# Kernel tuning notes

Hardware: AMD Instinct MI355X
Metric: run time of the kernel (lower is better)

Reference implementation:

```python
import jax, jax.numpy as jnp
import numpy as np

D_MODEL = 1024
SEQ = 4096
BATCH = 4


def _rope_cos_sin(m, d, dtype=jnp.float32):
    # Faithful to source: theta = 10000 ** (-2*(i-1)/d)  (note the i-1, as in the torch code)
    i = jnp.arange(d // 2, dtype=jnp.float32)
    theta = 10000.0 ** (-2.0 * (i - 1.0) / d)          # [d/2]
    ang = jnp.arange(m, dtype=jnp.float32)[:, None] * theta[None, :]  # [m, d/2]
    return jnp.cos(ang).astype(dtype), jnp.sin(ang).astype(dtype)


def _rotate(t, cos, sin):
    # t: [b, m, d]. Equivalent to (t @ R[pos]) with the source's block-diagonal R:
    # out[2i]   =  t[2i]*cos + t[2i+1]*sin
    # out[2i+1] = -t[2i]*sin + t[2i+1]*cos
    b, m, d = t.shape
    t2 = t.reshape(b, m, d // 2, 2)
    e, o = t2[..., 0], t2[..., 1]
    out = jnp.stack([e * cos + o * sin, -e * sin + o * cos], axis=-1)
    return out.reshape(b, m, d)


def setup_inputs() -> dict:
    key = jax.random.key(0)
    kx, kq, kk, kv = jax.random.split(key, 4)
    s = 1.0 / np.sqrt(D_MODEL)
    return {
        "x": jax.random.normal(kx, (BATCH, SEQ, D_MODEL), dtype=jnp.float32),
        "w_q": jax.random.normal(kq, (D_MODEL, D_MODEL), dtype=jnp.float32) * s,
        "w_k": jax.random.normal(kk, (D_MODEL, D_MODEL), dtype=jnp.float32) * s,
        "w_v": jax.random.normal(kv, (D_MODEL, D_MODEL), dtype=jnp.float32) * s,
    }


def reference(x, w_q, w_k, w_v):
    b, m, d = x.shape
    q = x @ w_q.T  # nn.Linear: y = x W^T
    k = x @ w_k.T
    v = x @ w_v.T
    cos, sin = _rope_cos_sin(m, d, x.dtype)
    q_rot = _rotate(q, cos, sin)
    k_rot = _rotate(k, cos, sin)
    # causal scaled dot-product attention (dropout disabled for deterministic reference)
    scale = 1.0 / jnp.sqrt(jnp.asarray(d, x.dtype))
    scores = jnp.einsum('bqd,bkd->bqk', q_rot, k_rot) * scale  # [b, m, m]
    causal = jnp.tril(jnp.ones((m, m), dtype=bool))
    scores = jnp.where(causal[None], scores, jnp.asarray(-jnp.inf, x.dtype))
    weights = jax.nn.softmax(scores, axis=-1)
    return jnp.einsum('bqk,bkd->bqd', weights, v)
```

## Files before the change

### kernel.cpp

```cpp
#include <hip/hip_runtime.h>

#define BATCH 4
#define SEQ 4096
#define DM 1024
#define HALF_D 512
#define NROWS (BATCH * SEQ)
#define NT128 528
#define TILE_ELE 16384

typedef _Float16 f16x8 __attribute__((ext_vector_type(8)));
typedef _Float16 f16x4 __attribute__((ext_vector_type(4)));
typedef _Float16 f16x2 __attribute__((ext_vector_type(2)));
typedef float f32x4 __attribute__((ext_vector_type(4)));

#define AS1(p) ((const __attribute__((address_space(1))) void*)(p))
#define AS3(p) ((__attribute__((address_space(3))) void*)(p))

__global__ __launch_bounds__(256) void cvt_f32_f16(
    const float* __restrict__ src, _Float16* __restrict__ dst, int n8) {
  int i = blockIdx.x * 256 + threadIdx.x;
  if (i >= n8) return;
  const float4* s = (const float4*)src;
  float4 a = s[2 * i], b = s[2 * i + 1];
  f16x8 h;
  h[0] = (_Float16)a.x; h[1] = (_Float16)a.y;
  h[2] = (_Float16)a.z; h[3] = (_Float16)a.w;
  h[4] = (_Float16)b.x; h[5] = (_Float16)b.y;
  h[6] = (_Float16)b.z; h[7] = (_Float16)b.w;
  *(f16x8*)&dst[8 * i] = h;
}

__global__ __launch_bounds__(256) void rope_apply(_Float16* __restrict__ T) {
  int idx = blockIdx.x * 256 + threadIdx.x;
  int row = idx >> 9;
  int i = idx & 511;
  int pos = row & (SEQ - 1);
  float theta = expf(-0.017988946039016f * ((float)i - 1.0f));
  float ang = (float)pos * theta;
  float c = cosf(ang), s = sinf(ang);
  f16x2 p = ((f16x2*)T)[idx];
  float e = (float)p[0], o = (float)p[1];
  p[0] = (_Float16)(e * c + o * s);
  p[1] = (_Float16)(o * c - e * s);
  ((f16x2*)T)[idx] = p;
}

template <int MODE>
__global__ __launch_bounds__(256) void gemm128(
    const _Float16* __restrict__ A, const _Float16* __restrict__ B,
    void* __restrict__ Cv, int K, int lda, int ldb, int ldc,
    long long strideA, long long strideB, long long strideC) {
  int bx = blockIdx.x, bz = blockIdx.z;
  int by = (MODE == 2) ? (31 - blockIdx.y) : blockIdx.y;
  if (MODE == 1 && bx > by) return;
  A += (size_t)bz * strideA;
  B += (size_t)bz * strideB;

  __shared__ __align__(16) _Float16 sA[128 * 64];
  __shared__ __align__(16) _Float16 sB[128 * 64];

  const int tid = threadIdx.x;
  const int lane = tid & 63, wave = tid >> 6;
  const int wm = (wave & 1) * 64, wn = (wave >> 1) * 64;
  const int r16 = lane & 15, quad = lane >> 4;
  const int m0 = by * 128, n0 = bx * 128;
  const int triBase = by * (by + 1) / 2;

  f32x4 acc[4][4] = {};

  const int nkt = (MODE == 2) ? (by + 1) * 2 : (K >> 6);

  for (int kt = 0; kt < nkt; ++kt) {
#pragma unroll
    for (int j = 0; j < 4; ++j) {
      int c = j * 256 + tid;
      int row = c >> 3, col = c & 7;
      const _Float16* gA;
      if (MODE == 2) {
        gA = A + (size_t)(triBase + (kt >> 1)) * TILE_ELE + row * 128 +
             (kt & 1) * 64 + col * 8;
      } else {
        gA = A + (size_t)(m0 + row) * lda + kt * 64 + col * 8;
      }
      const _Float16* gB = B + (size_t)(n0 + row) * ldb + kt * 64 + col * 8;
      __builtin_amdgcn_global_load_lds(AS1(gA), AS3(&sA[(j * 256 + wave * 64) * 8]), 16, 0, 0);
      __builtin_amdgcn_global_load_lds(AS1(gB), AS3(&sB[(j * 256 + wave * 64) * 8]), 16, 0, 0);
    }
    __syncthreads();

#pragma unroll
    for (int ks = 0; ks < 2; ++ks) {
      f16x8 af[4], bf[4];
#pragma unroll
      for (int i = 0; i < 4; ++i) {
        af[i] = *(const f16x8*)&sA[(wm + i * 16 + r16) * 64 + ks * 32 + quad * 8];
        bf[i] = *(const f16x8*)&sB[(wn + i * 16 + r16) * 64 + ks * 32 + quad * 8];
      }
#pragma unroll
      for (int mi = 0; mi < 4; ++mi)
#pragma unroll
        for (int ni = 0; ni < 4; ++ni)
          acc[mi][ni] = __builtin_amdgcn_mfma_f32_16x16x32_f16(
              af[mi], bf[ni], acc[mi][ni], 0, 0, 0);
    }
    __syncthreads();
  }

  if (MODE == 0) {
    _Float16* C = (_Float16*)Cv;
#pragma unroll
    for (int mi = 0; mi < 4; ++mi)
#pragma unroll
      for (int ni = 0; ni < 4; ++ni)
#pragma unroll
        for (int r = 0; r < 4; ++r) {
          int grow = m0 + wm + mi * 16 + quad * 4 + r;
          int gcol = n0 + wn + ni * 16 + r16;
          C[(size_t)grow * ldc + gcol] = (_Float16)acc[mi][ni][r];
        }
  } else if (MODE == 1) {
    _Float16* C = (_Float16*)Cv + (size_t)bz * strideC +
                  (size_t)(triBase + bx) * TILE_ELE;
#pragma unroll
    for (int mi = 0; mi < 4; ++mi)
#pragma unroll
      for (int ni = 0; ni < 4; ++ni)
#pragma unroll
        for (int r = 0; r < 4; ++r) {
          int lr = wm + mi * 16 + quad * 4 + r;
          int lc = wn + ni * 16 + r16;
          C[lr * 128 + lc] = (_Float16)(acc[mi][ni][r] * 0.03125f);
        }
  } else if (MODE == 2) {
    float* C = (float*)Cv + (size_t)bz * strideC;
#pragma unroll
    for (int mi = 0; mi < 4; ++mi)
#pragma unroll
      for (int ni = 0; ni < 4; ++ni)
#pragma unroll
        for (int r = 0; r < 4; ++r) {
          int grow = m0 + wm + mi * 16 + quad * 4 + r;
          int gcol = n0 + wn + ni * 16 + r16;
          C[(size_t)grow * ldc + gcol] = acc[mi][ni][r];
        }
  } else {
    _Float16* C = (_Float16*)Cv;
#pragma unroll
    for (int mi = 0; mi < 4; ++mi)
#pragma unroll
      for (int ni = 0; ni < 4; ++ni) {
        int gcol = n0 + wn + ni * 16 + r16;
        int growb = m0 + wm + mi * 16 + quad * 4;
        int b = growb >> 12;
        int m = growb & (SEQ - 1);
        f16x4 t;
#pragma unroll
        for (int r = 0; r < 4; ++r) t[r] = (_Float16)acc[mi][ni][r];
        *(f16x4*)&C[((size_t)b * DM + gcol) * SEQ + m] = t;
      }
  }
}

__global__ __launch_bounds__(256) void softmax_rows(_Float16* __restrict__ Sp) {
  __shared__ float vals[SEQ];
  __shared__ float red[256];
  int row = blockIdx.x;
  int b = row >> 12;
  int q = row & (SEQ - 1);
  int i = q >> 7, r = q & 127;
  _Float16* base = Sp + (size_t)b * ((size_t)NT128 * TILE_ELE) +
                   (size_t)(i * (i + 1) / 2) * TILE_ELE + (size_t)r * 128;
  int tid = threadIdx.x;
  int Kv = q + 1;
  float m = -__builtin_inff();
  for (int kb = tid * 8; kb + 8 <= Kv; kb += 2048) {
    f16x8 v8 = *(const f16x8*)&base[(kb >> 7) * TILE_ELE + (kb & 127)];
#pragma unroll
    for (int t = 0; t < 8; ++t) {
      float v = (float)v8[t];
      vals[kb + t] = v;
      m = fmaxf(m, v);
    }
  }
  if (tid == 0) {
    for (int k = Kv & ~7; k < Kv; ++k) {
      float v = (float)base[(k >> 7) * TILE_ELE + (k & 127)];
      vals[k] = v;
      m = fmaxf(m, v);
    }
  }
  red[tid] = m;
  __syncthreads();
  for (int s = 128; s > 0; s >>= 1) {
    if (tid < s) red[tid] = fmaxf(red[tid], red[tid + s]);
    __syncthreads();
  }
  m = red[0];
  __syncthreads();
  float l = 0.f;
  for (int k = tid; k < Kv; k += 256) {
    float e = __expf(vals[k] - m);
    vals[k] = e;
    l += e;
  }
  red[tid] = l;
  __syncthreads();
  for (int s = 128; s > 0; s >>= 1) {
    if (tid < s) red[tid] += red[tid + s];
    __syncthreads();
  }
  float inv = 1.0f / red[0];
  int Kend = (i + 1) * 128;
  for (int kb = tid * 8; kb < Kend; kb += 2048) {
    f16x8 p;
#pragma unroll
    for (int t = 0; t < 8; ++t) {
      int k = kb + t;
      p[t] = (k < Kv) ? (_Float16)(vals[k] * inv) : (_Float16)0.f;
    }
    *(f16x8*)&base[(kb >> 7) * TILE_ELE + (kb & 127)] = p;
  }
}

extern "C" void kernel_launch(void* const* d_in, const int* in_sizes, int n_in,
                              void* d_out, int out_size, void* d_ws,
                              size_t ws_size, hipStream_t stream) {
  const float* x = (const float*)d_in[0];
  const float* wq = (const float*)d_in[1];
  const float* wk = (const float*)d_in[2];
  const float* wv = (const float*)d_in[3];
  float* out = (float*)d_out;

  char* ws = (char*)d_ws;
  _Float16* Sp = (_Float16*)ws;
  _Float16* xh = (_Float16*)ws;
  _Float16* wqh = (_Float16*)(ws + 33554432);
  _Float16* wkh = wqh + (size_t)DM * DM;
  _Float16* wvh = wkh + (size_t)DM * DM;
  _Float16* vth = (_Float16*)(ws + 69206016);
  _Float16* qh = (_Float16*)d_out;
  _Float16* kh = qh + (size_t)NROWS * DM;
  (void)ws_size; (void)in_sizes; (void)n_in; (void)out_size;

  cvt_f32_f16<<<8192, 256, 0, stream>>>(x, xh, NROWS * DM / 8);
  cvt_f32_f16<<<512, 256, 0, stream>>>(wq, wqh, DM * DM / 8);
  cvt_f32_f16<<<512, 256, 0, stream>>>(wk, wkh, DM * DM / 8);
  cvt_f32_f16<<<512, 256, 0, stream>>>(wv, wvh, DM * DM / 8);

  dim3 g0(DM / 128, NROWS / 128, 1);
  gemm128<0><<<g0, 256, 0, stream>>>(xh, wqh, qh, DM, DM, DM, DM, 0, 0, 0);
  gemm128<0><<<g0, 256, 0, stream>>>(xh, wkh, kh, DM, DM, DM, DM, 0, 0, 0);
  gemm128<3><<<g0, 256, 0, stream>>>(xh, wvh, vth, DM, DM, DM, 0, 0, 0, 0);

  rope_apply<<<NROWS * HALF_D / 256, 256, 0, stream>>>(qh);
  rope_apply<<<NROWS * HALF_D / 256, 256, 0, stream>>>(kh);

  gemm128<1><<<dim3(SEQ / 128, SEQ / 128, BATCH), 256, 0, stream>>>(
      qh, kh, Sp, DM, DM, DM, 128, (long long)SEQ * DM, (long long)SEQ * DM,
      (long long)NT128 * TILE_ELE);

  softmax_rows<<<NROWS, 256, 0, stream>>>(Sp);

  gemm128<2><<<dim3(DM / 128, SEQ / 128, BATCH), 256, 0, stream>>>(
      Sp, vth, out, SEQ, 0, SEQ, DM, (long long)NT128 * TILE_ELE,
      (long long)DM * SEQ, (long long)SEQ * DM);
}
```

Measured before the change: 699.5 us.

## Register-prefetch GEMM tiles with XOR-swizzled LDS and compact triangular grid

Replaces direct global-to-LDS loads with register-staged loads. The next k-tile is fetched into registers while MFMAs run on the current tile, so global latency overlaps compute. LDS writes and reads use an XOR swizzle of the 16-byte chunk index to avoid bank conflicts on the fragment reads. The causal QK^T launch now maps a 1D block index to lower-triangle tiles instead of launching a full grid and exiting half the blocks. The cost is more registers per thread, which may lower occupancy.

```diff
diff --git a/kernel.cpp b/kernel.cpp
--- a/kernel.cpp
+++ b/kernel.cpp
@@ -12,9 +12,6 @@
 typedef _Float16 f16x4 __attribute__((ext_vector_type(4)));
 typedef _Float16 f16x2 __attribute__((ext_vector_type(2)));
 typedef float f32x4 __attribute__((ext_vector_type(4)));
-
-#define AS1(p) ((const __attribute__((address_space(1))) void*)(p))
-#define AS3(p) ((__attribute__((address_space(3))) void*)(p))
 
 __global__ __launch_bounds__(256) void cvt_f32_f16(
     const float* __restrict__ src, _Float16* __restrict__ dst, int n8) {
@@ -50,9 +47,18 @@
     const _Float16* __restrict__ A, const _Float16* __restrict__ B,
     void* __restrict__ Cv, int K, int lda, int ldb, int ldc,
     long long strideA, long long strideB, long long strideC) {
-  int bx = blockIdx.x, bz = blockIdx.z;
-  int by = (MODE == 2) ? (31 - blockIdx.y) : blockIdx.y;
-  if (MODE == 1 && bx > by) return;
+  int bx, by;
+  if (MODE == 1) {
+    int t = blockIdx.x;
+    by = (int)((sqrtf(8.0f * (float)t + 1.0f) - 1.0f) * 0.5f);
+    while ((by + 1) * (by + 2) / 2 <= t) ++by;
+    while (by * (by + 1) / 2 > t) --by;
+    bx = t - by * (by + 1) / 2;
+  } else {
+    bx = blockIdx.x;
+    by = (MODE == 2) ? (31 - blockIdx.y) : blockIdx.y;
+  }
+  int bz = blockIdx.z;
   A += (size_t)bz * strideA;
   B += (size_t)bz * strideB;
 
@@ -67,10 +73,11 @@
   const int triBase = by * (by + 1) / 2;
 
   f32x4 acc[4][4] = {};
+  int4 ra[4], rb[4];
 
   const int nkt = (MODE == 2) ? (by + 1) * 2 : (K >> 6);
 
-  for (int kt = 0; kt < nkt; ++kt) {
+  auto gload = [&](int kt) {
 #pragma unroll
     for (int j = 0; j < 4; ++j) {
       int c = j * 256 + tid;
@@ -83,18 +90,34 @@
         gA = A + (size_t)(m0 + row) * lda + kt * 64 + col * 8;
       }
       const _Float16* gB = B + (size_t)(n0 + row) * ldb + kt * 64 + col * 8;
-      __builtin_amdgcn_global_load_lds(AS1(gA), AS3(&sA[(j * 256 + wave * 64) * 8]), 16, 0, 0);
-      __builtin_amdgcn_global_load_lds(AS1(gB), AS3(&sB[(j * 256 + wave * 64) * 8]), 16, 0, 0);
-    }
-    __syncthreads();
+      ra[j] = *(const int4*)gA;
+      rb[j] = *(const int4*)gB;
+    }
+  };
+
+  gload(0);
+  for (int kt = 0; kt < nkt; ++kt) {
+#pragma unroll
+    for (int j = 0; j < 4; ++j) {
+      int c = j * 256 + tid;
+      int row = c >> 3, col = c & 7;
+      int lofs = row * 64 + ((col ^ (row & 7)) * 8);
+      *(int4*)&sA[lofs] = ra[j];
+      *(int4*)&sB[lofs] = rb[j];
+    }
+    __syncthreads();
+    if (kt + 1 < nkt) gload(kt + 1);
 
 #pragma unroll
     for (int ks = 0; ks < 2; ++ks) {
       f16x8 af[4], bf[4];
 #pragma unroll
       for (int i = 0; i < 4; ++i) {
-        af[i] = *(const f16x8*)&sA[(wm + i * 16 + r16) * 64 + ks * 32 + quad * 8];
-        bf[i] = *(const f16x8*)&sB[(wn + i * 16 + r16) * 64 + ks * 32 + quad * 8];
+        int rowA = wm + i * 16 + r16;
+        int rowB = wn + i * 16 + r16;
+        int chk = ((ks * 4 + quad) ^ (r16 & 7)) * 8;
+        af[i] = *(const f16x8*)&sA[rowA * 64 + chk];
+        bf[i] = *(const f16x8*)&sB[rowB * 64 + chk];
       }
 #pragma unroll
       for (int mi = 0; mi < 4; ++mi)
@@ -255,7 +278,7 @@
   rope_apply<<<NROWS * HALF_D / 256, 256, 0, stream>>>(qh);
   rope_apply<<<NROWS * HALF_D / 256, 256, 0, stream>>>(kh);
 
-  gemm128<1><<<dim3(SEQ / 128, SEQ / 128, BATCH), 256, 0, stream>>>(
+  gemm128<1><<<dim3(NT128, 1, BATCH), 256, 0, stream>>>(
       qh, kh, Sp, DM, DM, DM, 128, (long long)SEQ * DM, (long long)SEQ * DM,
       (long long)NT128 * TILE_ELE);
 
```

Result: slower. 1.464 ms (+109.3%).

## Store GEMM LDS tiles in MFMA fragment order and launch only causal QK tiles

Applied to the files above, without the earlier changes.

The LDS layout for the A and B tiles is reorganized so each wave's 16x32 MFMA fragment is stored contiguously, letting every lane read its f16x8 with a linear lane*8 offset. This is meant to remove the bank conflicts of the previous row-major 64-wide stride. The global loads are remapped to match, which makes them less contiguous per instruction. The QK^T launch is also changed to a 1D grid over the 528 lower-triangular tiles, with the tile indices recovered through a sqrt, so no blocks launch only to exit early.

```diff
diff --git a/kernel.cpp b/kernel.cpp
--- a/kernel.cpp
+++ b/kernel.cpp
@@ -50,14 +50,23 @@
     const _Float16* __restrict__ A, const _Float16* __restrict__ B,
     void* __restrict__ Cv, int K, int lda, int ldb, int ldc,
     long long strideA, long long strideB, long long strideC) {
-  int bx = blockIdx.x, bz = blockIdx.z;
-  int by = (MODE == 2) ? (31 - blockIdx.y) : blockIdx.y;
-  if (MODE == 1 && bx > by) return;
+  int bx, by;
+  if (MODE == 1) {
+    int t = blockIdx.x;
+    by = (int)((sqrtf(8.0f * (float)t + 1.0f) - 1.0f) * 0.5f);
+    while ((by + 1) * (by + 2) / 2 <= t) ++by;
+    while (by * (by + 1) / 2 > t) --by;
+    bx = t - by * (by + 1) / 2;
+  } else {
+    bx = blockIdx.x;
+    by = (MODE == 2) ? (31 - blockIdx.y) : blockIdx.y;
+  }
+  int bz = blockIdx.z;
   A += (size_t)bz * strideA;
   B += (size_t)bz * strideB;
 
-  __shared__ __align__(16) _Float16 sA[128 * 64];
-  __shared__ __align__(16) _Float16 sB[128 * 64];
+  __shared__ __align__(16) _Float16 sA[8192];
+  __shared__ __align__(16) _Float16 sB[8192];
 
   const int tid = threadIdx.x;
   const int lane = tid & 63, wave = tid >> 6;
@@ -73,18 +82,21 @@
   for (int kt = 0; kt < nkt; ++kt) {
 #pragma unroll
     for (int j = 0; j < 4; ++j) {
-      int c = j * 256 + tid;
-      int row = c >> 3, col = c & 7;
+      int blk = j * 4 + wave;
+      int i16 = blk & 7;
+      int ks = blk >> 3;
+      int row = i16 * 16 + r16;
+      int colh = ks * 32 + quad * 8;
       const _Float16* gA;
       if (MODE == 2) {
         gA = A + (size_t)(triBase + (kt >> 1)) * TILE_ELE + row * 128 +
-             (kt & 1) * 64 + col * 8;
+             (kt & 1) * 64 + colh;
       } else {
-        gA = A + (size_t)(m0 + row) * lda + kt * 64 + col * 8;
+        gA = A + (size_t)(m0 + row) * lda + kt * 64 + colh;
       }
-      const _Float16* gB = B + (size_t)(n0 + row) * ldb + kt * 64 + col * 8;
-      __builtin_amdgcn_global_load_lds(AS1(gA), AS3(&sA[(j * 256 + wave * 64) * 8]), 16, 0, 0);
-      __builtin_amdgcn_global_load_lds(AS1(gB), AS3(&sB[(j * 256 + wave * 64) * 8]), 16, 0, 0);
+      const _Float16* gB = B + (size_t)(n0 + row) * ldb + kt * 64 + colh;
+      __builtin_amdgcn_global_load_lds(AS1(gA), AS3(&sA[(size_t)blk * 512]), 16, 0, 0);
+      __builtin_amdgcn_global_load_lds(AS1(gB), AS3(&sB[(size_t)blk * 512]), 16, 0, 0);
     }
     __syncthreads();
 
@@ -93,8 +105,8 @@
       f16x8 af[4], bf[4];
 #pragma unroll
       for (int i = 0; i < 4; ++i) {
-        af[i] = *(const f16x8*)&sA[(wm + i * 16 + r16) * 64 + ks * 32 + quad * 8];
-        bf[i] = *(const f16x8*)&sB[(wn + i * 16 + r16) * 64 + ks * 32 + quad * 8];
+        af[i] = *(const f16x8*)&sA[ks * 4096 + ((wm >> 4) + i) * 512 + lane * 8];
+        bf[i] = *(const f16x8*)&sB[ks * 4096 + ((wn >> 4) + i) * 512 + lane * 8];
       }
 #pragma unroll
       for (int mi = 0; mi < 4; ++mi)
@@ -255,7 +267,7 @@
   rope_apply<<<NROWS * HALF_D / 256, 256, 0, stream>>>(qh);
   rope_apply<<<NROWS * HALF_D / 256, 256, 0, stream>>>(kh);
 
-  gemm128<1><<<dim3(SEQ / 128, SEQ / 128, BATCH), 256, 0, stream>>>(
+  gemm128<1><<<dim3(NT128, 1, BATCH), 256, 0, stream>>>(
       qh, kh, Sp, DM, DM, DM, 128, (long long)SEQ * DM, (long long)SEQ * DM,
       (long long)NT128 * TILE_ELE);
 
```

Result: slower. 749.7 us (+7.2%).
